# Performance work log

Hardware: AMD Instinct MI355X
Metric: run time of the kernel (lower is better)

The kernel has to match this reference:

```python
import jax, jax.numpy as jnp
import numpy as np
import math

B, S, IN, D, H = 128, 128, 16, 256, 256


def _gates(pre):
    i, f, g, o = jnp.split(pre, 4, axis=-1)
    return jax.nn.sigmoid(i), jax.nn.sigmoid(f), jnp.tanh(g), jax.nn.sigmoid(o)


def _lstm_dir(xp, Whh):
    # xp: [B,S,4H] precomputed input projection (+ both biases); scan over time.
    b = xp.shape[0]
    h_dim = Whh.shape[1]

    def step(carry, xt):
        h, c = carry
        i, f, g, o = _gates(xt + h @ Whh.T)
        c = f * c + i * g
        h = o * jnp.tanh(c)
        return (h, c), h

    init = (jnp.zeros((b, h_dim), xp.dtype), jnp.zeros((b, h_dim), xp.dtype))
    (hT, cT), hs = jax.lax.scan(step, init, jnp.swapaxes(xp, 0, 1))
    return jnp.swapaxes(hs, 0, 1), hT, cT


def _layernorm(x, g, b, eps=1e-5):
    m = jnp.mean(x, -1, keepdims=True)
    v = jnp.mean((x - m) ** 2, -1, keepdims=True)
    return (x - m) * jax.lax.rsqrt(v + eps) * g + b


def _forward(x, proj_W, proj_b, ln_g, ln_b,
             Wih_f, Whh_f, bih_f, bhh_f,
             Wih_b, Whh_b, bih_b, bhh_b,
             Wih_d, Whh_d, bih_d, bhh_d,
             hb_W, hb_b, cb_W, cb_b,
             gW1, gW2, gv, pW1, pW2, pv):
    b, s, _ = x.shape
    h_dim = Whh_d.shape[1]
    # Projector: Linear -> Tanh -> LayerNorm
    emb = _layernorm(jnp.tanh(x @ proj_W.T + proj_b), ln_g, ln_b)  # [B,S,D]
    # Bidirectional LSTM encoder (PyTorch gate order i,f,g,o)
    hf, hTf, cTf = _lstm_dir(emb @ Wih_f.T + (bih_f + bhh_f), Whh_f)
    hb_rev, hTb, cTb = _lstm_dir((emb @ Wih_b.T + (bih_b + bhh_b))[:, ::-1], Whh_b)
    hb_out = hb_rev[:, ::-1]
    enc = jnp.concatenate([hf, hb_out], -1)  # [B,S,2H]
    # Bridges to decoder init state
    h = jnp.tanh(jnp.concatenate([hTf, hTb], -1) @ hb_W.T + hb_b)
    c = jnp.tanh(jnp.concatenate([cTf, cTb], -1) @ cb_W.T + cb_b)
    dec_in = jnp.mean(enc, axis=1)  # [B,2H]
    # W1(encoder_outputs) is step-invariant: precompute once for both attentions
    g_ref = enc @ gW1.T  # [B,S,H]
    p_ref = enc @ pW1.T  # [B,S,H]
    scale = 1.0 / math.sqrt(h_dim)
    mask0 = jnp.zeros((b, s), jnp.bool_)

    def step(carry, _):
        h, c, mask, dec_in = carry
        # LSTMCell
        i, f, g, o = _gates(dec_in @ Wih_d.T + h @ Whh_d.T + bih_d + bhh_d)
        c = f * c + i * g
        h = o * jnp.tanh(c)
        # glimpse attention
        gs = jnp.tanh(g_ref + (h @ gW2.T)[:, None, :]) @ gv * scale  # [B,S]
        gp = jax.nn.softmax(jnp.where(mask, -1e9, gs), axis=1)
        ctx = jnp.einsum('bs,bsh->bh', gp, enc)  # [B,2H]
        # pointer attention (query = h + context[:, :H])
        ps = jnp.tanh(p_ref + ((h + ctx[:, :h_dim]) @ pW2.T)[:, None, :]) @ pv * scale
        ps = jnp.where(mask, -1e9, ps)  # masked scores are the returned logits
        sel = jnp.argmax(ps, axis=1)  # argmax(softmax(ps)) == argmax(ps)
        mask = mask | jax.nn.one_hot(sel, s, dtype=jnp.bool_)
        dec_in = jnp.take_along_axis(enc, sel[:, None, None], axis=1)[:, 0]
        return (h, c, mask, dec_in), (ps, sel)

    _, (logits, ptrs) = jax.lax.scan(step, (h, c, mask0, dec_in), None, length=s)
    return jnp.swapaxes(logits, 0, 1), jnp.swapaxes(ptrs, 0, 1)


def setup_inputs() -> dict:
    key = jax.random.key(0)
    ks = iter(jax.random.split(key, 20))

    def w(*shape):
        return jax.random.normal(next(ks), shape, jnp.float32) * 0.05

    z = lambda *shape: jnp.zeros(shape, jnp.float32)
    return {
        'x': jax.random.normal(next(ks), (B, S, IN), jnp.float32),
        'proj_W': w(D, IN), 'proj_b': z(D), 'ln_g': jnp.ones((D,), jnp.float32), 'ln_b': z(D),
        'Wih_f': w(4 * H, D), 'Whh_f': w(4 * H, H), 'bih_f': z(4 * H), 'bhh_f': z(4 * H),
        'Wih_b': w(4 * H, D), 'Whh_b': w(4 * H, H), 'bih_b': z(4 * H), 'bhh_b': z(4 * H),
        'Wih_d': w(4 * H, 2 * H), 'Whh_d': w(4 * H, H), 'bih_d': z(4 * H), 'bhh_d': z(4 * H),
        'hb_W': w(H, 2 * H), 'hb_b': z(H), 'cb_W': w(H, 2 * H), 'cb_b': z(H),
        'gW1': w(H, 2 * H), 'gW2': w(H, H), 'gv': w(H),
        'pW1': w(H, 2 * H), 'pW2': w(H, H), 'pv': w(H),
    }


def reference(x, proj_W, proj_b, ln_g, ln_b, Wih_f, Whh_f, bih_f, bhh_f, Wih_b, Whh_b, bih_b, bhh_b, Wih_d, Whh_d, bih_d, bhh_d, hb_W, hb_b, cb_W, cb_b, gW1, gW2, gv, pW1, pW2, pv):
    return _forward(x, proj_W, proj_b, ln_g, ln_b, Wih_f, Whh_f, bih_f, bhh_f, Wih_b, Whh_b, bih_b, bhh_b, Wih_d, Whh_d, bih_d, bhh_d, hb_W, hb_b, cb_W, cb_b, gW1, gW2, gv, pW1, pW2, pv)
```

## Files before the change

kernel.cpp:

```cpp
#include <hip/hip_runtime.h>
#include <cstdint>
#include <cstddef>

#define DEVINL __device__ __forceinline__

typedef float f32x4 __attribute__((ext_vector_type(4)));

DEVINL float ntload1(const float* p) {
    return __builtin_nontemporal_load(p);
}
DEVINL f32x4 ld4(const float* p) {
    return *reinterpret_cast<const f32x4*>(p);
}

DEVINL float frcp(float x) { return __builtin_amdgcn_rcpf(x); }
DEVINL float ftanh_fast(float x) {
    float e = __expf(2.0f * x);
    return 1.0f - 2.0f * frcp(e + 1.0f);
}
DEVINL float sig_precise(float x) { return 1.0f / (1.0f + expf(-x)); }
DEVINL float tanh_precise(float x) { return tanhf(x); }

#define BB 128
#define SS 128
#define IND 16
#define DD 256
#define HH 256
#define H4 1024
#define H2 512

__global__ __launch_bounds__(256) void k_proj_ln(
    const float* __restrict__ x, const float* __restrict__ projW,
    const float* __restrict__ projB, const float* __restrict__ ln_g,
    const float* __restrict__ ln_b, float* __restrict__ emb)
{
    __shared__ float Wl[256 * 17];
    __shared__ float xl[16];
    __shared__ float red[256];
    const int row = blockIdx.x;
    const int tid = threadIdx.x;
    for (int idx = tid; idx < 256 * 16; idx += 256) {
        int d = idx >> 4, i = idx & 15;
        Wl[d * 17 + i] = projW[idx];
    }
    if (tid < 16) xl[tid] = x[row * 16 + tid];
    __syncthreads();
    float acc = projB[tid];
#pragma unroll
    for (int i = 0; i < 16; ++i) acc = fmaf(Wl[tid * 17 + i], xl[i], acc);
    float v = tanh_precise(acc);
    red[tid] = v;
    __syncthreads();
    for (int s2 = 128; s2 > 0; s2 >>= 1) { if (tid < s2) red[tid] += red[tid + s2]; __syncthreads(); }
    float mean = red[0] * (1.0f / 256.0f);
    __syncthreads();
    float dlt = v - mean;
    red[tid] = dlt * dlt;
    __syncthreads();
    for (int s2 = 128; s2 > 0; s2 >>= 1) { if (tid < s2) red[tid] += red[tid + s2]; __syncthreads(); }
    float var = red[0] * (1.0f / 256.0f);
    float rs = 1.0f / sqrtf(var + 1e-5f);
    emb[(size_t)row * 256 + tid] = dlt * rs * ln_g[tid] + ln_b[tid];
}

__global__ __launch_bounds__(256) void k_gemm_nt(
    const float* __restrict__ A, int lda,
    const float* __restrict__ Bm,
    float* __restrict__ C,
    int M, int N, int K,
    const float* __restrict__ bias1, const float* __restrict__ bias2,
    int flags)
{
    __shared__ __align__(16) float As[16][132];
    __shared__ __align__(16) float Bs[16][132];
    const int tid = threadIdx.x;
    const int m0 = blockIdx.x * 128;
    const int n0 = blockIdx.y * 128;
    const int r = tid >> 1, half = tid & 1;
    const int tm = tid & 15, tn = tid >> 4;
    float acc[8][8];
#pragma unroll
    for (int i = 0; i < 8; ++i)
#pragma unroll
        for (int j = 0; j < 8; ++j) acc[i][j] = 0.0f;

    for (int k0 = 0; k0 < K; k0 += 16) {
        const float4* pa = reinterpret_cast<const float4*>(&A[(size_t)(m0 + r) * lda + k0 + half * 8]);
        float4 a0 = pa[0], a1 = pa[1];
        const float4* pb = reinterpret_cast<const float4*>(&Bm[(size_t)(n0 + r) * K + k0 + half * 8]);
        float4 b0 = pb[0], b1 = pb[1];
        __syncthreads();
        const int kb = half * 8;
        As[kb + 0][r] = a0.x; As[kb + 1][r] = a0.y; As[kb + 2][r] = a0.z; As[kb + 3][r] = a0.w;
        As[kb + 4][r] = a1.x; As[kb + 5][r] = a1.y; As[kb + 6][r] = a1.z; As[kb + 7][r] = a1.w;
        Bs[kb + 0][r] = b0.x; Bs[kb + 1][r] = b0.y; Bs[kb + 2][r] = b0.z; Bs[kb + 3][r] = b0.w;
        Bs[kb + 4][r] = b1.x; Bs[kb + 5][r] = b1.y; Bs[kb + 6][r] = b1.z; Bs[kb + 7][r] = b1.w;
        __syncthreads();
#pragma unroll
        for (int kk = 0; kk < 16; ++kk) {
            const float4 xa0 = *reinterpret_cast<const float4*>(&As[kk][tm * 8]);
            const float4 xa1 = *reinterpret_cast<const float4*>(&As[kk][tm * 8 + 4]);
            const float4 xb0 = *reinterpret_cast<const float4*>(&Bs[kk][tn * 8]);
            const float4 xb1 = *reinterpret_cast<const float4*>(&Bs[kk][tn * 8 + 4]);
            const float av[8] = {xa0.x, xa0.y, xa0.z, xa0.w, xa1.x, xa1.y, xa1.z, xa1.w};
            const float bv[8] = {xb0.x, xb0.y, xb0.z, xb0.w, xb1.x, xb1.y, xb1.z, xb1.w};
#pragma unroll
            for (int i = 0; i < 8; ++i)
#pragma unroll
                for (int j = 0; j < 8; ++j) acc[i][j] = fmaf(av[i], bv[j], acc[i][j]);
        }
    }
    const int nb = n0 + tn * 8;
    float bias[8];
#pragma unroll
    for (int j = 0; j < 8; ++j) {
        float bbv = 0.0f;
        if (bias1) bbv += bias1[nb + j];
        if (bias2) bbv += bias2[nb + j];
        bias[j] = bbv;
    }
#pragma unroll
    for (int i = 0; i < 8; ++i) {
        const size_t m = (size_t)(m0 + tm * 8 + i);
        float o[8];
#pragma unroll
        for (int j = 0; j < 8; ++j) {
            float vv = acc[i][j] + bias[j];
            if (flags & 1) vv = tanh_precise(vv);
            o[j] = vv;
        }
        float4* pc = reinterpret_cast<float4*>(&C[m * N + nb]);
        pc[0] = make_float4(o[0], o[1], o[2], o[3]);
        pc[1] = make_float4(o[4], o[5], o[6], o[7]);
    }
}

__global__ __launch_bounds__(512, 2) void k_lstm(
    const float* __restrict__ Whh_f, const float* __restrict__ Whh_b,
    const float* __restrict__ xf, const float* __restrict__ xb,
    float* __restrict__ enc, float* __restrict__ hT, float* __restrict__ cT)
{
    const int wg = blockIdx.x;
    const int dir = wg >> 7;
    const int bat = wg & 127;
    const float* W = dir ? Whh_b : Whh_f;
    const float* xin = dir ? xb : xf;
    const int tid = threadIdx.x;
    const int oct = tid & 7, jg = tid >> 3;

    __shared__ __align__(16) float h_lds[256];
    __shared__ float pre_lds[1024];

    if (tid < 256) h_lds[tid] = 0.0f;
    float c_reg = 0.0f;
    __syncthreads();

    for (int t = 0; t < SS; ++t) {
        const int st = dir ? (SS - 1 - t) : t;
        float hreg[32];
#pragma unroll
        for (int i = 0; i < 8; ++i) {
            f32x4 v = ld4(&h_lds[i * 32 + oct * 4]);
            hreg[i * 4 + 0] = v.x; hreg[i * 4 + 1] = v.y;
            hreg[i * 4 + 2] = v.z; hreg[i * 4 + 3] = v.w;
        }
        {
            f32x4 wA[8], wB[8];
            {
                const float* bp = &W[(size_t)jg * 256 + oct * 4];
#pragma unroll
                for (int i = 0; i < 8; ++i) wA[i] = ld4(bp + i * 32);
            }
            auto wstep = [&](f32x4 (&cur)[8], f32x4 (&nxt)[8], int q) {
                if (q < 15) {
                    const float* bp = &W[(size_t)((q + 1) * 64 + jg) * 256 + oct * 4];
#pragma unroll
                    for (int i = 0; i < 8; ++i) nxt[i] = ld4(bp + i * 32);
                }
                float a0 = 0.0f;
#pragma unroll
                for (int i = 0; i < 8; ++i) {
                    a0 = fmaf(cur[i].x, hreg[i * 4 + 0], a0);
                    a0 = fmaf(cur[i].y, hreg[i * 4 + 1], a0);
                    a0 = fmaf(cur[i].z, hreg[i * 4 + 2], a0);
                    a0 = fmaf(cur[i].w, hreg[i * 4 + 3], a0);
                }
                a0 += __shfl_xor(a0, 1); a0 += __shfl_xor(a0, 2); a0 += __shfl_xor(a0, 4);
                if (oct == 0) pre_lds[q * 64 + jg] = a0;
            };
#pragma unroll 1
            for (int q = 0; q < 16; q += 2) { wstep(wA, wB, q); wstep(wB, wA, q + 1); }
        }
        __syncthreads();
        if (tid < 256) {
            const int gc = tid;
            const float* xrow = &xin[((size_t)bat * SS + st) * 1024];
            float pi = pre_lds[gc]       + ntload1(&xrow[gc]);
            float pf = pre_lds[256 + gc] + ntload1(&xrow[256 + gc]);
            float pg = pre_lds[512 + gc] + ntload1(&xrow[512 + gc]);
            float po = pre_lds[768 + gc] + ntload1(&xrow[768 + gc]);
            float ig = sig_precise(pi), fg = sig_precise(pf);
            float gg = tanh_precise(pg), og = sig_precise(po);
            float cn = fmaf(fg, c_reg, ig * gg);
            float hn = og * tanh_precise(cn);
            c_reg = cn;
            h_lds[gc] = hn;
            enc[((size_t)bat * SS + st) * 512 + dir * 256 + gc] = hn;
            if (t == SS - 1) {
                hT[(size_t)bat * 512 + dir * 256 + gc] = hn;
                cT[(size_t)bat * 512 + dir * 256 + gc] = cn;
            }
        }
        __syncthreads();
    }
}

__global__ __launch_bounds__(256) void k_meanw(const float* __restrict__ encW, float* __restrict__ pre0)
{
    const int b = blockIdx.x;
    const int tid = threadIdx.x;
    const float4* base = reinterpret_cast<const float4*>(&encW[(size_t)b * SS * 1024]);
    float sx = 0.0f, sy = 0.0f, sz = 0.0f, sw = 0.0f;
    for (int s = 0; s < SS; ++s) {
        float4 v = base[s * 256 + tid];
        sx += v.x; sy += v.y; sz += v.z; sw += v.w;
    }
    float4* out = reinterpret_cast<float4*>(&pre0[(size_t)b * 1024]);
    out[tid] = make_float4(sx * (1.0f / 128.0f), sy * (1.0f / 128.0f), sz * (1.0f / 128.0f), sw * (1.0f / 128.0f));
}

__global__ __launch_bounds__(1024) void k_decoder(
    const float* __restrict__ Whh_d,
    const float* __restrict__ gW2, const float* __restrict__ pW2,
    const float* __restrict__ gv, const float* __restrict__ pv,
    const float* __restrict__ g_ref, const float* __restrict__ p_ref,
    const float* __restrict__ encP, const float* __restrict__ encW,
    const float* __restrict__ pre0, const float* __restrict__ h0,
    const float* __restrict__ c0,
    float* __restrict__ out_logits, float* __restrict__ out_ptrs)
{
    const int b = blockIdx.x;
    const int tid = threadIdx.x;
    const int oct = tid & 7, jg = tid >> 3;
    const int wid = tid >> 6, lane = tid & 63;

    __shared__ __align__(16) float h_lds[256];
    __shared__ float c_lds[256];
    __shared__ float pre_lds[1024];
    __shared__ float row_lds[1024];
    __shared__ __align__(16) float hgp[512];
    __shared__ __align__(16) float hp_lds[256];
    __shared__ __align__(16) float gv_lds[256];
    __shared__ __align__(16) float pv_lds[256];
    __shared__ float sc_arr[128];
    __shared__ float e_arr[128];
    __shared__ __align__(16) float hp_half[16][256];
    __shared__ int mask_lds[128];
    __shared__ int ulist[128];
    __shared__ int ucount_s;
    __shared__ float Z_s;
    __shared__ int sel_s;

    if (tid < 256) {
        gv_lds[tid] = gv[tid];
        pv_lds[tid] = pv[tid];
        h_lds[tid] = h0[(size_t)b * 256 + tid];
        c_lds[tid] = c0[(size_t)b * 256 + tid];
    }
    if (tid < 128) mask_lds[tid] = 0;
    if (tid == 0) sel_s = -1;
    const float* grefb = g_ref + (size_t)b * SS * 256;
    const float* prefb = p_ref + (size_t)b * SS * 256;
    const float* encPb = encP + (size_t)b * SS * 256;
    __syncthreads();

    for (int t = 0; t < SS; ++t) {
        {
            const int sel = sel_s;
            const float* src = (sel < 0) ? &pre0[(size_t)b * 1024]
                                         : &encW[((size_t)(b * SS + sel)) * 1024];
            row_lds[tid] = src[tid];
        }
        if (tid >= 128 && tid < 256) sc_arr[tid - 128] = -1e9f;
        if (tid < 64) {
            const unsigned long long lowmask = (1ull << lane) - 1ull;
            const bool u0 = (mask_lds[lane] == 0);
            const unsigned long long b0m = __ballot(u0);
            if (u0) ulist[__popcll(b0m & lowmask)] = lane;
            const bool u1 = (mask_lds[lane + 64] == 0);
            const unsigned long long b1m = __ballot(u1);
            const int c0 = __popcll(b0m);
            if (u1) ulist[c0 + __popcll(b1m & lowmask)] = lane + 64;
            if (lane == 0) ucount_s = c0 + __popcll(b1m);
        }
        float hreg[32];
#pragma unroll
        for (int i = 0; i < 8; ++i) {
            f32x4 v = ld4(&h_lds[i * 32 + oct * 4]);
            hreg[i * 4 + 0] = v.x; hreg[i * 4 + 1] = v.y;
            hreg[i * 4 + 2] = v.z; hreg[i * 4 + 3] = v.w;
        }
        __syncthreads();
        {
            f32x4 wA[8], wB[8];
            {
                const float* bp = &Whh_d[(size_t)jg * 256 + oct * 4];
#pragma unroll
                for (int i = 0; i < 8; ++i) wA[i] = ld4(bp + i * 32);
            }
            auto p1 = [&](f32x4 (&cur)[8], f32x4 (&nxt)[8], int q) {
                if (q < 7) {
                    const float* bp = &Whh_d[(size_t)((q + 1) * 128 + jg) * 256 + oct * 4];
#pragma unroll
                    for (int i = 0; i < 8; ++i) nxt[i] = ld4(bp + i * 32);
                }
                float a0 = 0.0f;
#pragma unroll
                for (int i = 0; i < 8; ++i) {
                    a0 = fmaf(cur[i].x, hreg[i * 4 + 0], a0);
                    a0 = fmaf(cur[i].y, hreg[i * 4 + 1], a0);
                    a0 = fmaf(cur[i].z, hreg[i * 4 + 2], a0);
                    a0 = fmaf(cur[i].w, hreg[i * 4 + 3], a0);
                }
                a0 += __shfl_xor(a0, 1); a0 += __shfl_xor(a0, 2); a0 += __shfl_xor(a0, 4);
                if (oct == 0) {
                    const int row = q * 128 + jg;
                    pre_lds[row] = a0 + row_lds[row];
                }
            };
#pragma unroll 1
            for (int q = 0; q < 8; q += 2) { p1(wA, wB, q); p1(wB, wA, q + 1); }
        }
        __syncthreads();
        if (tid < 256) {
            const int ch = tid;
            float pi = pre_lds[ch],        pf = pre_lds[256 + ch];
            float pg = pre_lds[512 + ch],  po = pre_lds[768 + ch];
            float ig = sig_precise(pi), fg = sig_precise(pf);
            float gg = tanh_precise(pg), og = sig_precise(po);
            float cn = fmaf(fg, c_lds[ch], ig * gg);
            float hn = og * tanh_precise(cn);
            c_lds[ch] = cn;
            h_lds[ch] = hn;
        }
        __syncthreads();
        float hreg2[32];
#pragma unroll
        for (int i = 0; i < 8; ++i) {
            f32x4 v = ld4(&h_lds[i * 32 + oct * 4]);
            hreg2[i * 4 + 0] = v.x; hreg2[i * 4 + 1] = v.y;
            hreg2[i * 4 + 2] = v.z; hreg2[i * 4 + 3] = v.w;
        }
        {
            f32x4 wA[8], wB[8];
            {
                const float* src0 = (jg < 256) ? &gW2[(size_t)jg * 256] : &pW2[(size_t)(jg - 256) * 256];
#pragma unroll
                for (int i = 0; i < 8; ++i) wA[i] = ld4(src0 + oct * 4 + i * 32);
            }
            auto p3 = [&](f32x4 (&cur)[8], f32x4 (&nxt)[8], int q) {
                if (q < 3) {
                    const int r2 = (q + 1) * 128 + jg;
                    const float* src = (r2 < 256) ? &gW2[(size_t)r2 * 256] : &pW2[(size_t)(r2 - 256) * 256];
#pragma unroll
                    for (int i = 0; i < 8; ++i) nxt[i] = ld4(src + oct * 4 + i * 32);
                }
                float a0 = 0.0f;
#pragma unroll
                for (int i = 0; i < 8; ++i) {
                    a0 = fmaf(cur[i].x, hreg2[i * 4 + 0], a0);
                    a0 = fmaf(cur[i].y, hreg2[i * 4 + 1], a0);
                    a0 = fmaf(cur[i].z, hreg2[i * 4 + 2], a0);
                    a0 = fmaf(cur[i].w, hreg2[i * 4 + 3], a0);
                }
                a0 += __shfl_xor(a0, 1); a0 += __shfl_xor(a0, 2); a0 += __shfl_xor(a0, 4);
                if (oct == 0) hgp[q * 128 + jg] = a0;
            };
#pragma unroll 1
            for (int q = 0; q < 4; q += 2) { p3(wA, wB, q); p3(wB, wA, q + 1); }
        }
        __syncthreads();
        {
            const int uc = ucount_s;
            if (jg < uc) {
                const int r = ulist[jg];
                const float* gr = &grefb[(size_t)r * 256 + oct * 4];
                f32x4 g0[8];
#pragma unroll
                for (int i = 0; i < 8; ++i) g0[i] = ld4(gr + i * 32);
                float part = 0.0f;
#pragma unroll
                for (int i = 0; i < 8; ++i) {
                    const int d = i * 32 + oct * 4;
                    const f32x4 hh = ld4(&hgp[d]);
                    const f32x4 vv = ld4(&gv_lds[d]);
                    part = fmaf(ftanh_fast(g0[i].x + hh.x), vv.x, part);
                    part = fmaf(ftanh_fast(g0[i].y + hh.y), vv.y, part);
                    part = fmaf(ftanh_fast(g0[i].z + hh.z), vv.z, part);
                    part = fmaf(ftanh_fast(g0[i].w + hh.w), vv.w, part);
                }
                part += __shfl_xor(part, 1); part += __shfl_xor(part, 2); part += __shfl_xor(part, 4);
                if (oct == 0) sc_arr[r] = part * 0.0625f;
            }
        }
        __syncthreads();
        if (tid < 64) {
            float s0 = sc_arr[lane], s1 = sc_arr[lane + 64];
            float m = fmaxf(s0, s1);
#pragma unroll
            for (int mk = 1; mk < 64; mk <<= 1) m = fmaxf(m, __shfl_xor(m, mk));
            float e0 = expf(s0 - m), e1 = expf(s1 - m);
            e_arr[lane] = e0; e_arr[lane + 64] = e1;
            float z = e0 + e1;
#pragma unroll
            for (int mk = 1; mk < 64; mk <<= 1) z += __shfl_xor(z, mk);
            if (lane == 0) Z_s = z;
        }
        __syncthreads();
        {
            const int uc = ucount_s;
            const int d4 = lane * 4;
            float ax = 0.0f, ay = 0.0f, az = 0.0f, aw = 0.0f;
            if (wid * 8 < uc) {
                f32x4 p0[8]; float ee[8];
#pragma unroll
                for (int i = 0; i < 8; ++i) {
                    const int k = wid * 8 + i;
                    const int kc = (k < uc) ? k : (uc - 1);
                    const int s = ulist[kc];
                    ee[i] = (k < uc) ? e_arr[s] : 0.0f;
                    p0[i] = ld4(&encPb[(size_t)s * 256 + d4]);
                }
#pragma unroll
                for (int i = 0; i < 8; ++i) {
                    ax = fmaf(p0[i].x, ee[i], ax); ay = fmaf(p0[i].y, ee[i], ay);
                    az = fmaf(p0[i].z, ee[i], az); aw = fmaf(p0[i].w, ee[i], aw);
                }
            }
            *reinterpret_cast<float4*>(&hp_half[wid][d4]) = make_float4(ax, ay, az, aw);
        }
        __syncthreads();
        if (tid < 256) {
            float s = 0.0f;
#pragma unroll
            for (int k = 0; k < 16; ++k) s += hp_half[k][tid];
            hp_lds[tid] = hgp[256 + tid] + s * frcp(Z_s);
        }
        __syncthreads();
        {
            const int uc = ucount_s;
            if (jg < uc) {
                const int r = ulist[jg];
                const float* pr = &prefb[(size_t)r * 256 + oct * 4];
                f32x4 g0[8];
#pragma unroll
                for (int i = 0; i < 8; ++i) g0[i] = ld4(pr + i * 32);
                float part = 0.0f;
#pragma unroll
                for (int i = 0; i < 8; ++i) {
                    const int d = i * 32 + oct * 4;
                    const f32x4 hh = ld4(&hp_lds[d]);
                    const f32x4 vv = ld4(&pv_lds[d]);
                    part = fmaf(ftanh_fast(g0[i].x + hh.x), vv.x, part);
                    part = fmaf(ftanh_fast(g0[i].y + hh.y), vv.y, part);
                    part = fmaf(ftanh_fast(g0[i].z + hh.z), vv.z, part);
                    part = fmaf(ftanh_fast(g0[i].w + hh.w), vv.w, part);
                }
                part += __shfl_xor(part, 1); part += __shfl_xor(part, 2); part += __shfl_xor(part, 4);
                if (oct == 0) sc_arr[r] = part * 0.0625f;
            }
        }
        __syncthreads();
        if (tid < 128) {
            out_logits[((size_t)(b * SS + t)) * SS + tid] = sc_arr[tid];
        }
        if (tid < 64) {
            float v = sc_arr[lane];
            int idx = lane;
            float v2 = sc_arr[lane + 64];
            if (v2 > v) { v = v2; idx = lane + 64; }
#pragma unroll
            for (int mk = 1; mk < 64; mk <<= 1) {
                float ov = __shfl_xor(v, mk);
                int oi = __shfl_xor(idx, mk);
                if (ov > v || (ov == v && oi < idx)) { v = ov; idx = oi; }
            }
            if (lane == 0) {
                sel_s = idx;
                mask_lds[idx] = 1;
                out_ptrs[(size_t)b * SS + t] = (float)idx;
            }
        }
        __syncthreads();
    }
}

extern "C" void kernel_launch(void* const* d_in, const int* in_sizes, int n_in,
                              void* d_out, int out_size, void* d_ws, size_t ws_size,
                              hipStream_t stream)
{
    (void)in_sizes; (void)n_in; (void)out_size; (void)ws_size;
    const float* x      = (const float*)d_in[0];
    const float* proj_W = (const float*)d_in[1];
    const float* proj_b = (const float*)d_in[2];
    const float* ln_g   = (const float*)d_in[3];
    const float* ln_b   = (const float*)d_in[4];
    const float* Wih_f  = (const float*)d_in[5];
    const float* Whh_f  = (const float*)d_in[6];
    const float* bih_f  = (const float*)d_in[7];
    const float* bhh_f  = (const float*)d_in[8];
    const float* Wih_b  = (const float*)d_in[9];
    const float* Whh_b  = (const float*)d_in[10];
    const float* bih_b  = (const float*)d_in[11];
    const float* bhh_b  = (const float*)d_in[12];
    const float* Wih_d  = (const float*)d_in[13];
    const float* Whh_d  = (const float*)d_in[14];
    const float* bih_d  = (const float*)d_in[15];
    const float* bhh_d  = (const float*)d_in[16];
    const float* hb_W   = (const float*)d_in[17];
    const float* hb_b   = (const float*)d_in[18];
    const float* cb_W   = (const float*)d_in[19];
    const float* cb_b   = (const float*)d_in[20];
    const float* gW1    = (const float*)d_in[21];
    const float* gW2    = (const float*)d_in[22];
    const float* gv     = (const float*)d_in[23];
    const float* pW1    = (const float*)d_in[24];
    const float* pW2    = (const float*)d_in[25];
    const float* pv     = (const float*)d_in[26];

    float* ws = (float*)d_ws;
    const size_t o_hT    = 0;
    const size_t o_cT    = 65536;
    const size_t o_h0    = 131072;
    const size_t o_c0    = 163840;
    const size_t o_pre0  = 196608;
    const size_t o_emb   = 0;
    const size_t o_xf    = 4194304;
    const size_t o_xb    = o_xf + 16777216;
    const size_t o_enc   = o_xb + 16777216;
    const size_t o_encW  = o_xf;
    const size_t o_gref  = o_xb;
    const size_t o_pref  = o_xb + 4194304;
    const size_t o_encP  = o_xb + 8388608;

    float* emb  = ws + o_emb;
    float* xf   = ws + o_xf;
    float* xb   = ws + o_xb;
    float* enc  = ws + o_enc;
    float* hT   = ws + o_hT;
    float* cT   = ws + o_cT;
    float* h0b  = ws + o_h0;
    float* c0b  = ws + o_c0;
    float* pre0 = ws + o_pre0;
    float* encW = ws + o_encW;
    float* gref = ws + o_gref;
    float* pref = ws + o_pref;
    float* encP = ws + o_encP;

    float* out_logits = (float*)d_out;
    float* out_ptrs   = out_logits + (size_t)BB * SS * SS;

    k_proj_ln<<<BB * SS, 256, 0, stream>>>(x, proj_W, proj_b, ln_g, ln_b, emb);
    {
        dim3 g(128, 8);
        k_gemm_nt<<<g, 256, 0, stream>>>(emb, 256, Wih_f, xf, 16384, 1024, 256, bih_f, bhh_f, 0);
        k_gemm_nt<<<g, 256, 0, stream>>>(emb, 256, Wih_b, xb, 16384, 1024, 256, bih_b, bhh_b, 0);
    }
    k_lstm<<<256, 512, 0, stream>>>(Whh_f, Whh_b, xf, xb, enc, hT, cT);
    {
        dim3 g(1, 2);
        k_gemm_nt<<<g, 256, 0, stream>>>(hT, 512, hb_W, h0b, 128, 256, 512, hb_b, nullptr, 1);
        k_gemm_nt<<<g, 256, 0, stream>>>(cT, 512, cb_W, c0b, 128, 256, 512, cb_b, nullptr, 1);
    }
    {
        dim3 g2(128, 2);
        k_gemm_nt<<<g2, 256, 0, stream>>>(enc, 512, gW1, gref, 16384, 256, 512, nullptr, nullptr, 0);
        k_gemm_nt<<<g2, 256, 0, stream>>>(enc, 512, pW1, pref, 16384, 256, 512, nullptr, nullptr, 0);
        dim3 g1(128, 8);
        k_gemm_nt<<<g1, 256, 0, stream>>>(enc, 512, Wih_d, encW, 16384, 1024, 512, bih_d, bhh_d, 0);
        k_gemm_nt<<<g2, 256, 0, stream>>>(enc, 512, pW2, encP, 16384, 256, 256, nullptr, nullptr, 0);
    }
    k_meanw<<<BB, 256, 0, stream>>>(encW, pre0);
    k_decoder<<<128, 1024, 0, stream>>>(Whh_d, gW2, pW2, gv, pv, gref, pref, encP, encW,
                                        pre0, h0b, c0b, out_logits, out_ptrs);
}
```

Measured before the change: 5.916 ms.

## Widen encoder LSTM blocks and fuse decoder Whh matvec with attention W2 pass

The encoder LSTM kernel now launches 1024 threads per block instead of 512, so each thread group handles 8 row-chunks of the recurrent matvec instead of 16, halving the per-step serial loop. In the decoder, the h·Whh_d product for the next step is computed right after h is updated, in the same streaming pass as the gW2/pW2 glimpse projections, with the initial product hoisted before the loop. This removes one barrier-separated matvec phase per decoder step. The trade-off is larger blocks with fewer waves of occupancy per CU, and the loop now also computes a Whh product on the last step that is never used.

```diff
diff --git a/kernel.cpp b/kernel.cpp
--- a/kernel.cpp
+++ b/kernel.cpp
@@ -135,7 +135,7 @@
     }
 }
 
-__global__ __launch_bounds__(512, 2) void k_lstm(
+__global__ __launch_bounds__(1024) void k_lstm(
     const float* __restrict__ Whh_f, const float* __restrict__ Whh_b,
     const float* __restrict__ xf, const float* __restrict__ xb,
     float* __restrict__ enc, float* __restrict__ hT, float* __restrict__ cT)
@@ -172,8 +172,8 @@
                 for (int i = 0; i < 8; ++i) wA[i] = ld4(bp + i * 32);
             }
             auto wstep = [&](f32x4 (&cur)[8], f32x4 (&nxt)[8], int q) {
-                if (q < 15) {
-                    const float* bp = &W[(size_t)((q + 1) * 64 + jg) * 256 + oct * 4];
+                if (q < 7) {
+                    const float* bp = &W[(size_t)((q + 1) * 128 + jg) * 256 + oct * 4];
 #pragma unroll
                     for (int i = 0; i < 8; ++i) nxt[i] = ld4(bp + i * 32);
                 }
@@ -186,10 +186,10 @@
                     a0 = fmaf(cur[i].w, hreg[i * 4 + 3], a0);
                 }
                 a0 += __shfl_xor(a0, 1); a0 += __shfl_xor(a0, 2); a0 += __shfl_xor(a0, 4);
-                if (oct == 0) pre_lds[q * 64 + jg] = a0;
+                if (oct == 0) pre_lds[q * 128 + jg] = a0;
             };
 #pragma unroll 1
-            for (int q = 0; q < 16; q += 2) { wstep(wA, wB, q); wstep(wB, wA, q + 1); }
+            for (int q = 0; q < 8; q += 2) { wstep(wA, wB, q); wstep(wB, wA, q + 1); }
         }
         __syncthreads();
         if (tid < 256) {
@@ -246,7 +246,7 @@
 
     __shared__ __align__(16) float h_lds[256];
     __shared__ float c_lds[256];
-    __shared__ float pre_lds[1024];
+    __shared__ float wacc_lds[1024];
     __shared__ float row_lds[1024];
     __shared__ __align__(16) float hgp[512];
     __shared__ __align__(16) float hp_lds[256];
@@ -274,6 +274,42 @@
     const float* encPb = encP + (size_t)b * SS * 256;
     __syncthreads();
 
+    {
+        float hreg0[32];
+#pragma unroll
+        for (int i = 0; i < 8; ++i) {
+            f32x4 v = ld4(&h_lds[i * 32 + oct * 4]);
+            hreg0[i * 4 + 0] = v.x; hreg0[i * 4 + 1] = v.y;
+            hreg0[i * 4 + 2] = v.z; hreg0[i * 4 + 3] = v.w;
+        }
+        f32x4 wA[8], wB[8];
+        {
+            const float* bp = &Whh_d[(size_t)jg * 256 + oct * 4];
+#pragma unroll
+            for (int i = 0; i < 8; ++i) wA[i] = ld4(bp + i * 32);
+        }
+        auto pw = [&](f32x4 (&cur)[8], f32x4 (&nxt)[8], int q) {
+            if (q < 7) {
+                const float* bp = &Whh_d[(size_t)((q + 1) * 128 + jg) * 256 + oct * 4];
+#pragma unroll
+                for (int i = 0; i < 8; ++i) nxt[i] = ld4(bp + i * 32);
+            }
+            float a0 = 0.0f;
+#pragma unroll
+            for (int i = 0; i < 8; ++i) {
+                a0 = fmaf(cur[i].x, hreg0[i * 4 + 0], a0);
+                a0 = fmaf(cur[i].y, hreg0[i * 4 + 1], a0);
+                a0 = fmaf(cur[i].z, hreg0[i * 4 + 2], a0);
+                a0 = fmaf(cur[i].w, hreg0[i * 4 + 3], a0);
+            }
+            a0 += __shfl_xor(a0, 1); a0 += __shfl_xor(a0, 2); a0 += __shfl_xor(a0, 4);
+            if (oct == 0) wacc_lds[q * 128 + jg] = a0;
+        };
+#pragma unroll 1
+        for (int q = 0; q < 8; q += 2) { pw(wA, wB, q); pw(wB, wA, q + 1); }
+    }
+    __syncthreads();
+
     for (int t = 0; t < SS; ++t) {
         {
             const int sel = sel_s;
@@ -293,49 +329,13 @@
             if (u1) ulist[c0 + __popcll(b1m & lowmask)] = lane + 64;
             if (lane == 0) ucount_s = c0 + __popcll(b1m);
         }
-        float hreg[32];
-#pragma unroll
-        for (int i = 0; i < 8; ++i) {
-            f32x4 v = ld4(&h_lds[i * 32 + oct * 4]);
-            hreg[i * 4 + 0] = v.x; hreg[i * 4 + 1] = v.y;
-            hreg[i * 4 + 2] = v.z; hreg[i * 4 + 3] = v.w;
-        }
-        __syncthreads();
-        {
-            f32x4 wA[8], wB[8];
-            {
-                const float* bp = &Whh_d[(size_t)jg * 256 + oct * 4];
-#pragma unroll
-                for (int i = 0; i < 8; ++i) wA[i] = ld4(bp + i * 32);
-            }
-            auto p1 = [&](f32x4 (&cur)[8], f32x4 (&nxt)[8], int q) {
-                if (q < 7) {
-                    const float* bp = &Whh_d[(size_t)((q + 1) * 128 + jg) * 256 + oct * 4];
-#pragma unroll
-                    for (int i = 0; i < 8; ++i) nxt[i] = ld4(bp + i * 32);
-                }
-                float a0 = 0.0f;
-#pragma unroll
-                for (int i = 0; i < 8; ++i) {
-                    a0 = fmaf(cur[i].x, hreg[i * 4 + 0], a0);
-                    a0 = fmaf(cur[i].y, hreg[i * 4 + 1], a0);
-                    a0 = fmaf(cur[i].z, hreg[i * 4 + 2], a0);
-                    a0 = fmaf(cur[i].w, hreg[i * 4 + 3], a0);
-                }
-                a0 += __shfl_xor(a0, 1); a0 += __shfl_xor(a0, 2); a0 += __shfl_xor(a0, 4);
-                if (oct == 0) {
-                    const int row = q * 128 + jg;
-                    pre_lds[row] = a0 + row_lds[row];
-                }
-            };
-#pragma unroll 1
-            for (int q = 0; q < 8; q += 2) { p1(wA, wB, q); p1(wB, wA, q + 1); }
-        }
         __syncthreads();
         if (tid < 256) {
             const int ch = tid;
-            float pi = pre_lds[ch],        pf = pre_lds[256 + ch];
-            float pg = pre_lds[512 + ch],  po = pre_lds[768 + ch];
+            float pi = wacc_lds[ch]       + row_lds[ch];
+            float pf = wacc_lds[256 + ch] + row_lds[256 + ch];
+            float pg = wacc_lds[512 + ch] + row_lds[512 + ch];
+            float po = wacc_lds[768 + ch] + row_lds[768 + ch];
             float ig = sig_precise(pi), fg = sig_precise(pf);
             float gg = tanh_precise(pg), og = sig_precise(po);
             float cn = fmaf(fg, c_lds[ch], ig * gg);
@@ -344,40 +344,50 @@
             h_lds[ch] = hn;
         }
         __syncthreads();
-        float hreg2[32];
+        float hreg[32];
 #pragma unroll
         for (int i = 0; i < 8; ++i) {
             f32x4 v = ld4(&h_lds[i * 32 + oct * 4]);
-            hreg2[i * 4 + 0] = v.x; hreg2[i * 4 + 1] = v.y;
-            hreg2[i * 4 + 2] = v.z; hreg2[i * 4 + 3] = v.w;
+            hreg[i * 4 + 0] = v.x; hreg[i * 4 + 1] = v.y;
+            hreg[i * 4 + 2] = v.z; hreg[i * 4 + 3] = v.w;
         }
         {
             f32x4 wA[8], wB[8];
             {
-                const float* src0 = (jg < 256) ? &gW2[(size_t)jg * 256] : &pW2[(size_t)(jg - 256) * 256];
-#pragma unroll
-                for (int i = 0; i < 8; ++i) wA[i] = ld4(src0 + oct * 4 + i * 32);
-            }
-            auto p3 = [&](f32x4 (&cur)[8], f32x4 (&nxt)[8], int q) {
-                if (q < 3) {
-                    const int r2 = (q + 1) * 128 + jg;
-                    const float* src = (r2 < 256) ? &gW2[(size_t)r2 * 256] : &pW2[(size_t)(r2 - 256) * 256];
-#pragma unroll
-                    for (int i = 0; i < 8; ++i) nxt[i] = ld4(src + oct * 4 + i * 32);
+                const float* bp = &Whh_d[(size_t)jg * 256 + oct * 4];
+#pragma unroll
+                for (int i = 0; i < 8; ++i) wA[i] = ld4(bp + i * 32);
+            }
+            auto pm = [&](f32x4 (&cur)[8], f32x4 (&nxt)[8], int q) {
+                if (q < 11) {
+                    const int qn = q + 1;
+                    const float* bp;
+                    if (qn < 8) {
+                        bp = &Whh_d[(size_t)(qn * 128 + jg) * 256 + oct * 4];
+                    } else {
+                        const int r2 = (qn - 8) * 128 + jg;
+                        bp = (r2 < 256) ? &gW2[(size_t)r2 * 256 + oct * 4]
+                                        : &pW2[(size_t)(r2 - 256) * 256 + oct * 4];
+                    }
+#pragma unroll
+                    for (int i = 0; i < 8; ++i) nxt[i] = ld4(bp + i * 32);
                 }
                 float a0 = 0.0f;
 #pragma unroll
                 for (int i = 0; i < 8; ++i) {
-                    a0 = fmaf(cur[i].x, hreg2[i * 4 + 0], a0);
-                    a0 = fmaf(cur[i].y, hreg2[i * 4 + 1], a0);
-                    a0 = fmaf(cur[i].z, hreg2[i * 4 + 2], a0);
-                    a0 = fmaf(cur[i].w, hreg2[i * 4 + 3], a0);
+                    a0 = fmaf(cur[i].x, hreg[i * 4 + 0], a0);
+                    a0 = fmaf(cur[i].y, hreg[i * 4 + 1], a0);
+                    a0 = fmaf(cur[i].z, hreg[i * 4 + 2], a0);
+                    a0 = fmaf(cur[i].w, hreg[i * 4 + 3], a0);
                 }
                 a0 += __shfl_xor(a0, 1); a0 += __shfl_xor(a0, 2); a0 += __shfl_xor(a0, 4);
-                if (oct == 0) hgp[q * 128 + jg] = a0;
+                if (oct == 0) {
+                    if (q < 8) wacc_lds[q * 128 + jg] = a0;
+                    else       hgp[(q - 8) * 128 + jg] = a0;
+                }
             };
 #pragma unroll 1
-            for (int q = 0; q < 4; q += 2) { p3(wA, wB, q); p3(wB, wA, q + 1); }
+            for (int q = 0; q < 12; q += 2) { pm(wA, wB, q); pm(wB, wA, q + 1); }
         }
         __syncthreads();
         {
@@ -566,7 +576,7 @@
         k_gemm_nt<<<g, 256, 0, stream>>>(emb, 256, Wih_f, xf, 16384, 1024, 256, bih_f, bhh_f, 0);
         k_gemm_nt<<<g, 256, 0, stream>>>(emb, 256, Wih_b, xb, 16384, 1024, 256, bih_b, bhh_b, 0);
     }
-    k_lstm<<<256, 512, 0, stream>>>(Whh_f, Whh_b, xf, xb, enc, hT, cT);
+    k_lstm<<<256, 1024, 0, stream>>>(Whh_f, Whh_b, xf, xb, enc, hT, cT);
     {
         dim3 g(1, 2);
         k_gemm_nt<<<g, 256, 0, stream>>>(hT, 512, hb_W, h0b, 128, 256, 512, hb_b, nullptr, 1);
```

Result: slower. 6.301 ms (+6.5%).
